# Optimization experiments

Measured on AMD Instinct MI355X. Metric: run time of the kernel, lower is better.

## Reference

```python
import jax, jax.numpy as jnp
import numpy as np

# pywt db2 decomposition filters
DEC_LO = np.array([-0.12940952255092145, 0.22414386804185735,
                   0.836516303737469, 0.48296291314469025], dtype=np.float32)
DEC_HI = np.array([-0.48296291314469025, 0.836516303737469,
                   -0.22414386804185735, -0.12940952255092145], dtype=np.float32)

# pywt WaveletPacket2D.get_level(2, order='freq') graycode order over per-axis
# band paths: ['ll','lh','hh','hl'] -> (band at level1, band at level2), 0=low,1=high
GRAY = [(0, 0), (0, 1), (1, 1), (1, 0)]


def _pdwt_last(x, filts):
    """Single-level periodization-mode DWT along last axis.
    pywt 'per' mode (even N): out[i] = sum_j f[j] * x[(2i+1-j) mod N].
    Equivalent to circular left-pad by L-2 then VALID strided conv with the
    time-reversed filter. filts: [2, L] already reversed (lo, hi).
    Returns [..., 2, N//2] (band axis inserted before halved axis)."""
    *lead, N = x.shape
    L = filts.shape[-1]
    xe = jnp.concatenate([x[..., N - (L - 2):], x], axis=-1)  # [..., N+L-2]
    y = jax.lax.conv_general_dilated(
        xe.reshape(-1, 1, N + L - 2), filts[:, None, :],
        window_strides=(2,), padding='VALID')  # [B, 2, N//2]
    return y.reshape(*lead, 2, N // 2)


def _dwt2(x, filts):
    """2D single-level periodized DWT on the last two axes.
    x: [..., H, W] -> [..., 2(row band), 2(col band), H/2, W/2].
    Row band 1 = high-pass along axis -2 (pywt 'h' node = cH = 'da')."""
    y = _pdwt_last(x.swapaxes(-1, -2), filts)      # [..., W, 2, H/2]
    y = jnp.moveaxis(y, -2, -3).swapaxes(-1, -2)   # [..., 2, H/2, W]
    z = _pdwt_last(y, filts)                       # [..., 2, H/2, 2, W/2]
    return jnp.moveaxis(z, -2, -3)                 # [..., 2, 2, H/2, W/2]


def setup_inputs() -> dict:
    key = jax.random.key(0)
    x = jax.random.uniform(key, (3, 2048, 2048), dtype=jnp.float32)  # CHW in [0,1]
    return {"x": x, "dec_lo": jnp.asarray(DEC_LO), "dec_hi": jnp.asarray(DEC_HI)}


def reference(x, dec_lo, dec_hi):
    filts = jnp.stack([dec_lo[::-1], dec_hi[::-1]])  # time-reversed lo/hi, [2, L]
    b1 = _dwt2(x, filts)    # [C, 2, 2, H/2, W/2]            (r1, c1)
    b2 = _dwt2(b1, filts)   # [C, 2, 2, 2, 2, H/4, W/4]      (r1, c1, r2, c2)
    C = x.shape[0]
    h, w = b2.shape[-2:]
    # frequency-ordered 4x4 grid, flattened row-major, channels outermost
    bands = [b2[:, r1, c1, r2, c2] for (r1, r2) in GRAY for (c1, c2) in GRAY]
    y = jnp.stack(bands, axis=1)  # [C, 16, H/4, W/4]
    return y.reshape(C * 16, h, w)
```

## Files before the change

kernel.cpp:

```cpp
#include <hip/hip_runtime.h>

#define HH 2048
#define WW 2048
#define OH 512
#define OW 512
#define TKC 32
#define TKR 16
#define ROWS 70
#define PITCHF 144
#define V4PR 36
#define NV4 (ROWS * V4PR)
#define NBLK 512
#define TPB 3

#define BAR()    __builtin_amdgcn_s_barrier()
#define SCHED0() __builtin_amdgcn_sched_barrier(0)
#define WAITV(n) asm volatile("s_waitcnt vmcnt(" #n ")" ::: "memory")

__device__ __forceinline__ float rfl(float v) {
    return __int_as_float(__builtin_amdgcn_readfirstlane(__float_as_int(v)));
}

__global__ __launch_bounds__(512, 4)
void wpt2_kernel(const float* __restrict__ x,
                 const float* __restrict__ dec_lo,
                 const float* __restrict__ dec_hi,
                 float* __restrict__ out) {
    __shared__ float bufA[NV4 * 4];
    __shared__ float bufB[NV4 * 4];

    const int tx  = threadIdx.x;
    const int ty  = threadIdx.y;
    const int tid = ty * TKC + tx;

    const int bid = blockIdx.x;
    const int swz = (bid & 7) * (NBLK / 8) + (bid >> 3);
    const int tile0 = swz * TPB;

    float lo[4], hi[4];
#pragma unroll
    for (int j = 0; j < 4; ++j) { lo[j] = dec_lo[j]; hi[j] = dec_hi[j]; }
    float F[4][10];
#pragma unroll
    for (int g = 0; g < 4; ++g) {
        const float* f1 = (g >= 2) ? hi : lo;
        const float* f2 = (g == 1 || g == 2) ? hi : lo;
#pragma unroll
        for (int d = 0; d < 10; ++d) F[g][d] = 0.f;
#pragma unroll
        for (int j2 = 0; j2 < 4; ++j2)
#pragma unroll
            for (int j1 = 0; j1 < 4; ++j1)
                F[g][2 * j2 + j1] = fmaf(f2[j2], f1[j1], F[g][2 * j2 + j1]);
    }
#pragma unroll
    for (int g = 0; g < 4; ++g)
#pragma unroll
        for (int d = 0; d < 10; ++d) F[g][d] = rfl(F[g][d]);

    auto stage = [&](float* dst, int tileId) {
        const int ch  = tileId >> 9;
        const int rem = tileId & 511;
        const int tcc = rem >> 5;
        const int trr = rem & 31;
        const float* xc = x + (size_t)ch * HH * WW;
        const int r0 = 64 * trr - 6;
        const int c0 = 128 * tcc - 16;
#pragma unroll
        for (int j = 0; j < 5; ++j) {
            const int i = j * 512 + tid;
            if (j < 4 || i < NV4) {
                const int rr = i / V4PR;
                const int vc = i - rr * V4PR;
                int gr = r0 + rr;      if (gr < 0) gr += HH;
                int gc = c0 + 4 * vc;  if (gc < 0) gc += WW;
                __builtin_amdgcn_global_load_lds(
                    (const __attribute__((address_space(1))) void*)&xc[(size_t)gr * WW + gc],
                    (__attribute__((address_space(3))) void*)&dst[i * 4],
                    16, 0, 0);
            }
        }
    };

    auto compute = [&](const float* buf, int tileId) {
        const int ch  = tileId >> 9;
        const int rem = tileId & 511;
        const int tcc = rem >> 5;
        const int trr = rem & 31;

        __builtin_amdgcn_s_setprio(1);
        float t[4][10];
#pragma unroll
        for (int g = 0; g < 4; ++g)
#pragma unroll
            for (int d = 0; d < 10; ++d) t[g][d] = 0.f;

#pragma unroll
        for (int u = 0; u < 10; ++u) {
            const float* rp = &buf[(4 * ty + u) * PITCHF + 4 * tx + 8];
            const float4 a = *reinterpret_cast<const float4*>(rp);
            const float4 b = *reinterpret_cast<const float4*>(rp + 4);
            const float4 c = *reinterpret_cast<const float4*>(rp + 8);
            const float row[12] = {a.x, a.y, a.z, a.w, b.x, b.y, b.z, b.w,
                                   c.x, c.y, c.z, c.w};
            const int dr = 9 - u;
#pragma unroll
            for (int dc = 0; dc < 10; ++dc) {
                const float v = row[11 - dc];
#pragma unroll
                for (int g = 0; g < 4; ++g)
                    t[g][dc] = fmaf(F[g][dr], v, t[g][dc]);
            }
        }

        const int kr = TKR * trr + ty;
        const int kc = TKC * tcc + tx;
        const size_t plane = (size_t)OH * OW;
        float* op = out + (size_t)(ch * 16) * plane + (size_t)kr * OW + kc;
#pragma unroll
        for (int gi = 0; gi < 4; ++gi) {
#pragma unroll
            for (int gj = 0; gj < 4; ++gj) {
                float acc = 0.f;
#pragma unroll
                for (int dc = 0; dc < 10; ++dc)
                    acc = fmaf(F[gj][dc], t[gi][dc], acc);
                __builtin_nontemporal_store(acc, op + (size_t)(gi * 4 + gj) * plane);
            }
        }
        __builtin_amdgcn_s_setprio(0);
    };

    stage(bufA, tile0 + 0);
    WAITV(0);  BAR(); SCHED0();
    stage(bufB, tile0 + 1); compute(bufA, tile0 + 0);
    WAITV(16); BAR(); SCHED0();
    stage(bufA, tile0 + 2); compute(bufB, tile0 + 1);
    WAITV(16); BAR(); SCHED0();
    compute(bufA, tile0 + 2);
}

extern "C" void kernel_launch(void* const* d_in, const int* in_sizes, int n_in,
                              void* d_out, int out_size, void* d_ws, size_t ws_size,
                              hipStream_t stream) {
    const float* x      = (const float*)d_in[0];
    const float* dec_lo = (const float*)d_in[1];
    const float* dec_hi = (const float*)d_in[2];
    float* out          = (float*)d_out;

    hipLaunchKernelGGL(wpt2_kernel, dim3(NBLK), dim3(TKC, TKR), 0, stream,
                       x, dec_lo, dec_hi, out);
}
```

Measured before the change: 24.68 us.

## Apply row filter in registers before LDS, column pass on filtered data

```diff
diff --git a/kernel.cpp b/kernel.cpp
--- a/kernel.cpp
+++ b/kernel.cpp
@@ -6,16 +6,16 @@
 #define OW 512
 #define TKC 32
 #define TKR 16
-#define ROWS 70
-#define PITCHF 144
-#define V4PR 36
-#define NV4 (ROWS * V4PR)
+#define SROWS 70
+#define SSZ (SROWS * TKC * 4)
+#define NPAIR (SROWS * TKC)
 #define NBLK 512
 #define TPB 3
 
-#define BAR()    __builtin_amdgcn_s_barrier()
-#define SCHED0() __builtin_amdgcn_sched_barrier(0)
-#define WAITV(n) asm volatile("s_waitcnt vmcnt(" #n ")" ::: "memory")
+#define BAR()     __builtin_amdgcn_s_barrier()
+#define SCHED0()  __builtin_amdgcn_sched_barrier(0)
+#define WAITV(n)  asm volatile("s_waitcnt vmcnt(" #n ")" ::: "memory")
+#define WAITLGKM() asm volatile("s_waitcnt lgkmcnt(0)" ::: "memory")
 
 __device__ __forceinline__ float rfl(float v) {
     return __int_as_float(__builtin_amdgcn_readfirstlane(__float_as_int(v)));
@@ -26,8 +26,8 @@
                  const float* __restrict__ dec_lo,
                  const float* __restrict__ dec_hi,
                  float* __restrict__ out) {
-    __shared__ float bufA[NV4 * 4];
-    __shared__ float bufB[NV4 * 4];
+    __shared__ float sA[SSZ];
+    __shared__ float sB[SSZ];
 
     const int tx  = threadIdx.x;
     const int ty  = threadIdx.y;
@@ -58,58 +58,78 @@
 #pragma unroll
         for (int d = 0; d < 10; ++d) F[g][d] = rfl(F[g][d]);
 
-    auto stage = [&](float* dst, int tileId) {
+    auto gload = [&](float4 st[5][3], int tileId) {
         const int ch  = tileId >> 9;
         const int rem = tileId & 511;
         const int tcc = rem >> 5;
         const int trr = rem & 31;
         const float* xc = x + (size_t)ch * HH * WW;
-        const int r0 = 64 * trr - 6;
-        const int c0 = 128 * tcc - 16;
 #pragma unroll
-        for (int j = 0; j < 5; ++j) {
-            const int i = j * 512 + tid;
-            if (j < 4 || i < NV4) {
-                const int rr = i / V4PR;
-                const int vc = i - rr * V4PR;
-                int gr = r0 + rr;      if (gr < 0) gr += HH;
-                int gc = c0 + 4 * vc;  if (gc < 0) gc += WW;
-                __builtin_amdgcn_global_load_lds(
-                    (const __attribute__((address_space(1))) void*)&xc[(size_t)gr * WW + gc],
-                    (__attribute__((address_space(3))) void*)&dst[i * 4],
-                    16, 0, 0);
+        for (int k = 0; k < 5; ++k) {
+            const int p = k * 512 + tid;
+            if (k < 4 || p < NPAIR) {
+                const int r  = p >> 5;
+                const int kc = p & 31;
+                int grow = 64 * trr - 6 + r;  if (grow < 0) grow += HH;
+                const float* rp = xc + (size_t)grow * WW;
+                const int cb = 128 * tcc + 4 * kc;
+                int c0 = cb - 8;  if (c0 < 0) c0 += WW;
+                int c1 = cb - 4;  if (c1 < 0) c1 += WW;
+                st[k][0] = *reinterpret_cast<const float4*>(rp + c0);
+                st[k][1] = *reinterpret_cast<const float4*>(rp + c1);
+                st[k][2] = *reinterpret_cast<const float4*>(rp + cb);
             }
         }
     };
 
-    auto compute = [&](const float* buf, int tileId) {
+    auto rowfilt = [&](const float4 st[5][3], float* sbuf) {
+#pragma unroll
+        for (int k = 0; k < 5; ++k) {
+            const int p = k * 512 + tid;
+            if (k < 4 || p < NPAIR) {
+                const float w[12] = {st[k][0].x, st[k][0].y, st[k][0].z, st[k][0].w,
+                                     st[k][1].x, st[k][1].y, st[k][1].z, st[k][1].w,
+                                     st[k][2].x, st[k][2].y, st[k][2].z, st[k][2].w};
+                float s0 = 0.f, s1 = 0.f, s2 = 0.f, s3 = 0.f;
+#pragma unroll
+                for (int dc = 0; dc < 10; ++dc) {
+                    const float v = w[11 - dc];
+                    s0 = fmaf(F[0][dc], v, s0);
+                    s1 = fmaf(F[1][dc], v, s1);
+                    s2 = fmaf(F[2][dc], v, s2);
+                    s3 = fmaf(F[3][dc], v, s3);
+                }
+                float4 sv; sv.x = s0; sv.y = s1; sv.z = s2; sv.w = s3;
+                *reinterpret_cast<float4*>(&sbuf[p * 4]) = sv;
+            }
+        }
+    };
+
+    auto colpass = [&](const float* sbuf, int tileId) {
         const int ch  = tileId >> 9;
         const int rem = tileId & 511;
         const int tcc = rem >> 5;
         const int trr = rem & 31;
 
         __builtin_amdgcn_s_setprio(1);
-        float t[4][10];
+        float acc[4][4];
 #pragma unroll
-        for (int g = 0; g < 4; ++g)
+        for (int gi = 0; gi < 4; ++gi)
 #pragma unroll
-            for (int d = 0; d < 10; ++d) t[g][d] = 0.f;
+            for (int gj = 0; gj < 4; ++gj) acc[gi][gj] = 0.f;
 
 #pragma unroll
         for (int u = 0; u < 10; ++u) {
-            const float* rp = &buf[(4 * ty + u) * PITCHF + 4 * tx + 8];
-            const float4 a = *reinterpret_cast<const float4*>(rp);
-            const float4 b = *reinterpret_cast<const float4*>(rp + 4);
-            const float4 c = *reinterpret_cast<const float4*>(rp + 8);
-            const float row[12] = {a.x, a.y, a.z, a.w, b.x, b.y, b.z, b.w,
-                                   c.x, c.y, c.z, c.w};
+            const float4 sv = *reinterpret_cast<const float4*>(
+                &sbuf[((4 * ty + u) * TKC + tx) * 4]);
             const int dr = 9 - u;
 #pragma unroll
-            for (int dc = 0; dc < 10; ++dc) {
-                const float v = row[11 - dc];
-#pragma unroll
-                for (int g = 0; g < 4; ++g)
-                    t[g][dc] = fmaf(F[g][dr], v, t[g][dc]);
+            for (int gi = 0; gi < 4; ++gi) {
+                const float fr = F[gi][dr];
+                acc[gi][0] = fmaf(fr, sv.x, acc[gi][0]);
+                acc[gi][1] = fmaf(fr, sv.y, acc[gi][1]);
+                acc[gi][2] = fmaf(fr, sv.z, acc[gi][2]);
+                acc[gi][3] = fmaf(fr, sv.w, acc[gi][3]);
             }
         }
 
@@ -118,26 +138,34 @@
         const size_t plane = (size_t)OH * OW;
         float* op = out + (size_t)(ch * 16) * plane + (size_t)kr * OW + kc;
 #pragma unroll
-        for (int gi = 0; gi < 4; ++gi) {
+        for (int gi = 0; gi < 4; ++gi)
 #pragma unroll
-            for (int gj = 0; gj < 4; ++gj) {
-                float acc = 0.f;
-#pragma unroll
-                for (int dc = 0; dc < 10; ++dc)
-                    acc = fmaf(F[gj][dc], t[gi][dc], acc);
-                __builtin_nontemporal_store(acc, op + (size_t)(gi * 4 + gj) * plane);
-            }
-        }
+            for (int gj = 0; gj < 4; ++gj)
+                __builtin_nontemporal_store(acc[gi][gj],
+                                            op + (size_t)(gi * 4 + gj) * plane);
         __builtin_amdgcn_s_setprio(0);
     };
 
-    stage(bufA, tile0 + 0);
-    WAITV(0);  BAR(); SCHED0();
-    stage(bufB, tile0 + 1); compute(bufA, tile0 + 0);
-    WAITV(16); BAR(); SCHED0();
-    stage(bufA, tile0 + 2); compute(bufB, tile0 + 1);
-    WAITV(16); BAR(); SCHED0();
-    compute(bufA, tile0 + 2);
+    float4 st[5][3];
+
+    gload(st, tile0 + 0);
+    WAITV(0);
+    rowfilt(st, sA);
+    WAITLGKM(); BAR(); SCHED0();
+
+    gload(st, tile0 + 1); SCHED0();
+    colpass(sA, tile0 + 0);
+    WAITV(16);
+    rowfilt(st, sB);
+    WAITLGKM(); BAR(); SCHED0();
+
+    gload(st, tile0 + 2); SCHED0();
+    colpass(sB, tile0 + 1);
+    WAITV(16);
+    rowfilt(st, sA);
+    WAITLGKM(); BAR(); SCHED0();
+
+    colpass(sA, tile0 + 2);
 }
 
 extern "C" void kernel_launch(void* const* d_in, const int* in_sizes, int n_in,
```

Measured after the change: 21.51 us, median of 2. -12.8%, faster.
